# Performance work log

Measured on AMD Instinct MI355X. Metric: run time of the kernel, lower is better.

Reference implementation:

```python
import jax, jax.numpy as jnp
import numpy as np

GRID_SIZE, SPLINE_ORDER = 5, 3
NUM_BASES = GRID_SIZE + SPLINE_ORDER  # 8
GRID = jnp.asarray(np.arange(-SPLINE_ORDER, GRID_SIZE + SPLINE_ORDER + 1, dtype=np.float32) * (2.0 / GRID_SIZE) - 1.0)  # (12,)


def _b_splines(x):
    # x: (M, F) -> (M, F, NUM_BASES), Cox-de Boor recursion on shared uniform grid
    g = GRID
    xe = x[..., None]
    b = ((xe >= g[:-1]) & (xe < g[1:])).astype(x.dtype)
    for k in range(1, SPLINE_ORDER + 1):
        b = ((xe - g[:-(k + 1)]) / (g[k:-1] - g[:-(k + 1)]) * b[..., :-1]
             + (g[k + 1:] - xe) / (g[k + 1:] - g[1:-k]) * b[..., 1:])
    return b


def _kan_linear(x, base_w, spline_w):
    # x: (M, Fin); base_w: (Fout, Fin); spline_w: (Fout, Fin, NUM_BASES)
    base = jax.nn.silu(x) @ base_w.T
    spl = _b_splines(x).reshape(x.shape[0], -1) @ spline_w.reshape(spline_w.shape[0], -1).T
    return base + spl


def _ln(x, g, b, eps=1e-5):
    mu = jnp.mean(x, -1, keepdims=True)
    var = jnp.var(x, -1, keepdims=True)
    return (x - mu) * jax.lax.rsqrt(var + eps) * g + b


def _dwconv(img, w, b):
    C = img.shape[1]
    out = jax.lax.conv_general_dilated(img, w, (1, 1), 'SAME',
        dimension_numbers=('NCHW', 'OIHW', 'NCHW'), feature_group_count=C)
    return out + b[None, :, None, None]


def _dw_bn_relu(x, H, W, w, b, gamma, beta, eps=1e-5):
    # BN in eval mode with running_mean=0, running_var=1
    B, N, C = x.shape
    img = x.transpose(0, 2, 1).reshape(B, C, H, W)
    out = _dwconv(img, w, b)
    out = out * (gamma * (1.0 / np.sqrt(1.0 + eps)))[None, :, None, None] + beta[None, :, None, None]
    out = jax.nn.relu(out)
    return out.reshape(B, C, H * W).transpose(0, 2, 1)


def _cross_selective_scan(img, x_proj_w, dt_w, dt_b, A_logs, Ds, g, b):
    # img: (B, Di, H, W). 4-direction diagonal/antidiagonal selective scan (VMamba-style).
    B, Di, H, W = img.shape
    L = H * W
    K = x_proj_w.shape[0]
    R = dt_w.shape[2]
    Nst = A_logs.shape[1]
    i = jnp.arange(H)[:, None]
    j = jnp.arange(W)[None, :]
    diag = (i + j) % W
    adiag = (j - i) % W
    diag_inv = (jnp.arange(W)[None, :] - i) % W
    adiag_inv = (jnp.arange(W)[None, :] + i) % W

    def gather(x, idx):
        gth = jnp.take_along_axis(x, idx[None, None], axis=3)  # (B,Di,H,W)
        return gth.transpose(0, 1, 3, 2).reshape(B, Di, L)

    def scatter(flat, idx_inv):
        v = flat.reshape(B, Di, W, H).transpose(0, 1, 3, 2)
        return jnp.take_along_axis(v, idx_inv[None, None], axis=3)

    gd, gad = gather(img, diag), gather(img, adiag)
    xs = jnp.stack([gd, gad, jnp.flip(gd, -1), jnp.flip(gad, -1)], axis=1)  # (B,K,Di,L)
    x_dbl = jnp.einsum('bkdl,kcd->bkcl', xs, x_proj_w)
    dts, Bs, Cs = jnp.split(x_dbl, [R, R + Nst], axis=2)  # (B,K,R,L),(B,K,N,L),(B,K,N,L)
    dts = jnp.einsum('bkrl,kdr->bkdl', dts, dt_w)
    delta = jax.nn.softplus(dts + dt_b[None, :, :, None])  # (B,K,Di,L)
    A = -jnp.exp(A_logs).reshape(K, Di, Nst)

    def step(hst, inp):
        u_t, d_t, B_t, C_t = inp  # (B,K,Di),(B,K,Di),(B,K,N),(B,K,N)
        dA = jnp.exp(d_t[..., None] * A)
        hst = dA * hst + (d_t * u_t)[..., None] * B_t[:, :, None, :]
        return hst, jnp.einsum('bkdn,bkn->bkd', hst, C_t)

    h0 = jnp.zeros((B, K, Di, Nst), img.dtype)
    _, ys = jax.lax.scan(step, h0,
        (xs.transpose(3, 0, 1, 2), delta.transpose(3, 0, 1, 2),
         Bs.transpose(3, 0, 1, 2), Cs.transpose(3, 0, 1, 2)))  # ys: (L,B,K,Di)
    ys = ys.transpose(1, 2, 3, 0) + Ds.reshape(K, Di)[None, :, :, None] * xs  # (B,K,Di,L)
    yd = ys[:, 0] + jnp.flip(ys[:, 2], -1)
    ya = ys[:, 1] + jnp.flip(ys[:, 3], -1)
    y = scatter(yd, diag_inv) + scatter(ya, adiag_inv)  # (B,Di,H,W)
    y = y.reshape(B, Di, L).transpose(0, 2, 1)
    return _ln(y, g, b)  # (B,L,Di)


def setup_inputs():
    key = jax.random.key(0)
    ks = iter(jax.random.split(key, 48))
    B, H, W, C = 4, 64, 64, 96
    Di, K, Nst = 2 * C, 4, 16
    R = int(np.ceil(C / 16))
    L = H * W

    def rn(shape, s=0.05):
        return jax.random.normal(next(ks), shape, jnp.float32) * s

    return dict(
        x=jax.random.normal(next(ks), (B, L, C), jnp.float32),
        H=H, W=W,
        norm1_g=jnp.ones((C,), jnp.float32), norm1_b=jnp.zeros((C,), jnp.float32),
        in_proj_w=rn((2 * Di, C)),
        conv_w=rn((Di, 1, 3, 3), 0.2), conv_b=jnp.zeros((Di,), jnp.float32),
        x_proj_w=rn((K, R + 2 * Nst, Di)),
        dt_w=rn((K, Di, R), 0.1), dt_b=rn((K, Di), 0.1),
        A_logs=jax.random.uniform(next(ks), (K * Di, Nst), jnp.float32),
        Ds=jnp.ones((K * Di,), jnp.float32),
        out_norm_g=jnp.ones((Di,), jnp.float32), out_norm_b=jnp.zeros((Di,), jnp.float32),
        out_proj_w=rn((C, Di)),
        norm2_g=jnp.ones((C,), jnp.float32), norm2_b=jnp.zeros((C,), jnp.float32),
        fc1_base_w=rn((C, C)), fc1_spline_w=rn((C, C, NUM_BASES), 0.02),
        fc2_base_w=rn((C, C)), fc2_spline_w=rn((C, C, NUM_BASES), 0.02),
        fc3_base_w=rn((C, C)), fc3_spline_w=rn((C, C, NUM_BASES), 0.02),
        dw1_w=rn((C, 1, 3, 3), 0.2), dw1_b=jnp.zeros((C,), jnp.float32),
        dw1_g=jnp.ones((C,), jnp.float32), dw1_beta=jnp.zeros((C,), jnp.float32),
        dw2_w=rn((C, 1, 3, 3), 0.2), dw2_b=jnp.zeros((C,), jnp.float32),
        dw2_g=jnp.ones((C,), jnp.float32), dw2_beta=jnp.zeros((C,), jnp.float32),
        dw3_w=rn((C, 1, 3, 3), 0.2), dw3_b=jnp.zeros((C,), jnp.float32),
        dw3_g=jnp.ones((C,), jnp.float32), dw3_beta=jnp.zeros((C,), jnp.float32),
    )


def reference(x, H, W, norm1_g, norm1_b, in_proj_w, conv_w, conv_b, x_proj_w,
              dt_w, dt_b, A_logs, Ds, out_norm_g, out_norm_b, out_proj_w,
              norm2_g, norm2_b, fc1_base_w, fc1_spline_w, fc2_base_w, fc2_spline_w,
              fc3_base_w, fc3_spline_w, dw1_w, dw1_b, dw1_g, dw1_beta,
              dw2_w, dw2_b, dw2_g, dw2_beta, dw3_w, dw3_b, dw3_g, dw3_beta):
    B, L, C = x.shape
    # --- SS2D branch ---
    h = _ln(x, norm1_g, norm1_b)
    xz = h @ in_proj_w.T  # (B,L,2*Di)
    Di = xz.shape[-1] // 2
    xin, z = xz[..., :Di], xz[..., Di:]
    img = xin.transpose(0, 2, 1).reshape(B, Di, H, W)
    img = jax.nn.silu(_dwconv(img, conv_w, conv_b))
    y = _cross_selective_scan(img, x_proj_w, dt_w, dt_b, A_logs, Ds, out_norm_g, out_norm_b)
    y = y * jax.nn.silu(z)
    x = x + y @ out_proj_w.T
    # --- KAN branch ---
    h = _ln(x, norm2_g, norm2_b)
    M = B * L
    t = _kan_linear(h.reshape(M, C), fc1_base_w, fc1_spline_w).reshape(B, L, -1)
    t = _dw_bn_relu(t, H, W, dw1_w, dw1_b, dw1_g, dw1_beta)
    t = _kan_linear(t.reshape(M, -1), fc2_base_w, fc2_spline_w).reshape(B, L, -1)
    t = _dw_bn_relu(t, H, W, dw2_w, dw2_b, dw2_g, dw2_beta)
    t = _kan_linear(t.reshape(M, -1), fc3_base_w, fc3_spline_w).reshape(B, L, -1)
    t = _dw_bn_relu(t, H, W, dw3_w, dw3_b, dw3_g, dw3_beta)
    return x + t
```

## Files before the change

kernel.cpp:

```cpp
#include <hip/hip_runtime.h>
#include <math.h>

constexpr int B_  = 4;
constexpr int H_  = 64;
constexpr int W_  = 64;
constexpr int C_  = 96;
constexpr int L_  = H_ * W_;
constexpr int DI  = 192;
constexpr int K_  = 4;
constexpr int NST = 16;
constexpr int R_  = 6;
constexpr int M_  = B_ * L_;

constexpr int NCH = 128;
constexpr int CL  = 32;
constexpr int DG  = 12;
constexpr int HS  = 8;

constexpr int KANK = 864;
constexpr int KLAY = 96 * KANK;

typedef __attribute__((ext_vector_type(8))) short short8;
typedef __attribute__((ext_vector_type(4))) float floatx4;
typedef __attribute__((ext_vector_type(4))) unsigned short ushort4v;

__device__ __forceinline__ float wave_sum64(float v) {
#pragma unroll
  for (int off = 1; off < 64; off <<= 1) v += __shfl_xor(v, off, 64);
  return v;
}

__device__ __forceinline__ float exp2_hw(float x) {
  return __builtin_amdgcn_exp2f(x);
}

__device__ __forceinline__ int pos_kl(int k, int l) {
  int ll = (k >= 2) ? (L_ - 1 - l) : l;
  int i = ll & 63;
  int j = ll >> 6;
  int col = ((k & 1) == 0) ? ((i + j) & 63) : ((j - i) & 63);
  return (i << 6) + col;
}

__device__ __forceinline__ int pos_pair(int pr, int ll) {
  int i = ll & 63, j = ll >> 6;
  int col = (pr == 0) ? ((i + j) & 63) : ((j - i) & 63);
  return (i << 6) + col;
}

__device__ __forceinline__ float silu_f(float x) {
  return x / (1.f + __expf(-x));
}

__device__ __forceinline__ float softplus_fast(float s) {
  return fmaxf(s, 0.f) + __logf(1.f + __expf(-fabsf(s)));
}

__device__ __forceinline__ unsigned short f2bf(float f) {
  unsigned u = __float_as_uint(f);
  unsigned r = (u + 0x7FFFu + ((u >> 16) & 1u)) >> 16;
  return (unsigned short)r;
}

__device__ __forceinline__ float bf2f(unsigned short h) {
  return __uint_as_float(((unsigned)h) << 16);
}

__device__ __forceinline__ void spline8(float x, float* bb ) {
#pragma unroll
  for (int i2 = 0; i2 < 11; i2++) {
    float g0 = 0.4f * i2 - 2.2f;
    float g1 = 0.4f * i2 - 1.8f;
    bb[i2] = (x >= g0 && x < g1) ? 1.f : 0.f;
  }
#pragma unroll
  for (int k2 = 1; k2 <= 3; k2++) {
    float invd = 1.f / (0.4f * k2);
#pragma unroll
    for (int i2 = 0; i2 + k2 < 11; i2++) {
      float gi   = 0.4f * i2 - 2.2f;
      float gik1 = 0.4f * (i2 + k2 + 1) - 2.2f;
      bb[i2] = (x - gi) * invd * bb[i2] + (gik1 - x) * invd * bb[i2 + 1];
    }
  }
}

__global__ __launch_bounds__(256) void ln96_kernel(const float* __restrict__ in,
    const float* __restrict__ g, const float* __restrict__ b,
    float* __restrict__ out) {
  int wave = blockIdx.x * 4 + (threadIdx.x >> 6);
  int lane = threadIdx.x & 63;
  const float* rp = in + (size_t)wave * C_;
  float v0 = rp[lane];
  float v1 = (lane < C_ - 64) ? rp[lane + 64] : 0.f;
  float s  = wave_sum64(v0 + v1);
  float s2 = wave_sum64(v0 * v0 + v1 * v1);
  float mean = s * (1.f / C_);
  float var  = s2 * (1.f / C_) - mean * mean;
  float inv  = rsqrtf(var + 1e-5f);
  float* op = out + (size_t)wave * C_;
  op[lane] = (v0 - mean) * inv * g[lane] + b[lane];
  if (lane < C_ - 64) op[lane + 64] = (v1 - mean) * inv * g[lane + 64] + b[lane + 64];
}

__global__ __launch_bounds__(256) void prep_inproj_kernel(const float* __restrict__ w,
    unsigned short* __restrict__ wio) {
  int idx = blockIdx.x * 256 + threadIdx.x;
  if (idx >= 384 * 96) return;
  float v = w[idx];
  unsigned short hh = f2bf(v);
  wio[idx] = hh;
  wio[36864 + idx] = f2bf(v - bf2f(hh));
}

__global__ __launch_bounds__(256) void prep_a2_kernel(const float* __restrict__ A_logs,
    float* __restrict__ a2g) {
  int idx = blockIdx.x * 256 + threadIdx.x;
  if (idx < K_ * DI * NST) a2g[idx] = -__expf(A_logs[idx]) * 1.44269504f;
}

__global__ __launch_bounds__(256) void gemm_in_mfma_kernel(const float* __restrict__ h,
    const unsigned short* __restrict__ wio, float* __restrict__ xin,
    float* __restrict__ z) {
  __shared__ __align__(16) unsigned short Wh[96][104];
  __shared__ __align__(16) unsigned short Wl[96][104];
  int row0 = (blockIdx.x >> 1) * 64;
  int nc0  = (blockIdx.x & 1) * 2;
  int tid = threadIdx.x;
  int wv = tid >> 6, lane = tid & 63, mrow = lane & 15, quad = lane >> 4;

  short8 ah[3], al[3];
  const float* hr = h + (size_t)(row0 + wv * 16 + mrow) * C_;
#pragma unroll
  for (int ks = 0; ks < 3; ks++) {
    float4 va = *(const float4*)&hr[ks * 32 + quad * 8];
    float4 vb = *(const float4*)&hr[ks * 32 + quad * 8 + 4];
    float f[8] = {va.x, va.y, va.z, va.w, vb.x, vb.y, vb.z, vb.w};
    short8 hh, ll;
#pragma unroll
    for (int q = 0; q < 8; q++) {
      unsigned short hv = f2bf(f[q]);
      hh[q] = (short)hv;
      ll[q] = (short)f2bf(f[q] - bf2f(hv));
    }
    ah[ks] = hh; al[ks] = ll;
  }
  for (int nci = 0; nci < 2; nci++) {
    int nc = nc0 + nci;
    if (nci) __syncthreads();
    for (int t = tid; t < 96 * 12; t += 256) {
      int j = t / 12, u = t % 12;
      *(short8*)&Wh[j][u * 8] = *(const short8*)&wio[(size_t)(nc * 96 + j) * 96 + u * 8];
      *(short8*)&Wl[j][u * 8] = *(const short8*)&wio[(size_t)(384 + nc * 96 + j) * 96 + u * 8];
    }
    __syncthreads();
    floatx4 acc[6];
#pragma unroll
    for (int q = 0; q < 6; q++) acc[q] = (floatx4)(0.f);
#pragma unroll
    for (int ks = 0; ks < 3; ks++) {
#pragma unroll
      for (int nt = 0; nt < 6; nt++) {
        short8 bh = *(const short8*)&Wh[nt * 16 + mrow][ks * 32 + quad * 8];
        short8 bl = *(const short8*)&Wl[nt * 16 + mrow][ks * 32 + quad * 8];
        acc[nt] = __builtin_amdgcn_mfma_f32_16x16x32_bf16(ah[ks], bh, acc[nt], 0, 0, 0);
        acc[nt] = __builtin_amdgcn_mfma_f32_16x16x32_bf16(al[ks], bh, acc[nt], 0, 0, 0);
        acc[nt] = __builtin_amdgcn_mfma_f32_16x16x32_bf16(ah[ks], bl, acc[nt], 0, 0, 0);
      }
    }
#pragma unroll
    for (int nt = 0; nt < 6; nt++) {
      int j = nc * 96 + nt * 16 + mrow;
#pragma unroll
      for (int rg = 0; rg < 4; rg++) {
        int row = row0 + wv * 16 + quad * 4 + rg;
        float v = acc[nt][rg];
        if (j < DI) xin[(size_t)row * DI + j] = v;
        else        z[(size_t)row * DI + (j - DI)] = v;
      }
    }
  }
}

__global__ __launch_bounds__(192) void conv_silu_kernel(const float* __restrict__ xin,
    const float* __restrict__ cw, const float* __restrict__ cb, float* __restrict__ imgT) {
  int p = blockIdx.x;
  int b = p >> 12;
  int ij = p & 4095;
  int i = ij >> 6, j = ij & 63;
  int c = threadIdx.x;
  float acc = cb[c];
#pragma unroll
  for (int di = -1; di <= 1; di++) {
    int ii = i + di;
    if (ii < 0 || ii >= H_) continue;
#pragma unroll
    for (int dj = -1; dj <= 1; dj++) {
      int jj = j + dj;
      if (jj < 0 || jj >= W_) continue;
      acc += xin[((size_t)b * L_ + ii * W_ + jj) * DI + c] * cw[c * 9 + (di + 1) * 3 + (dj + 1)];
    }
  }
  imgT[(size_t)p * DI + c] = silu_f(acc);
}

__global__ __launch_bounds__(256) void xdbl_mfma_kernel(const float* __restrict__ imgT,
    const float* __restrict__ xpw, float* __restrict__ dts_g,
    float* __restrict__ BsT, float* __restrict__ CsT) {
  __shared__ __align__(16) unsigned short Ah[64][104];
  __shared__ __align__(16) unsigned short Al[64][104];
  __shared__ __align__(16) unsigned short Wh[48][104];
  __shared__ __align__(16) unsigned short Wl[48][104];
  __shared__ int pos_s[64];

  int blk = blockIdx.x;
  int lt = blk & 63;
  int bk = blk >> 6;
  int k = bk % K_, b = bk / K_;
  int l0 = lt * 64;
  int tid = threadIdx.x;
  int wid = tid >> 6;
  int lane = tid & 63;
  int mrow = lane & 15, quad = lane >> 4;

  if (tid < 64) pos_s[tid] = pos_kl(k, l0 + tid);
  __syncthreads();

  floatx4 acc[3];
#pragma unroll
  for (int q = 0; q < 3; q++) acc[q] = (floatx4)(0.f);

  const float* img_b = imgT + (size_t)b * L_ * DI;

  for (int kc = 0; kc < 2; kc++) {
    if (kc) __syncthreads();
    for (int t = tid; t < 64 * 24; t += 256) {
      int li = t / 24, c4 = (t % 24) * 4;
      const float4 v = *(const float4*)&img_b[(size_t)pos_s[li] * DI + kc * 96 + c4];
      ushort4v h4, l4;
      float fv[4] = {v.x, v.y, v.z, v.w};
#pragma unroll
      for (int q = 0; q < 4; q++) {
        unsigned short hh = f2bf(fv[q]);
        h4[q] = hh;
        l4[q] = f2bf(fv[q] - bf2f(hh));
      }
      *(ushort4v*)&Ah[li][c4] = h4;
      *(ushort4v*)&Al[li][c4] = l4;
    }
    for (int t = tid; t < 48 * 24; t += 256) {
      int j = t / 24, c4 = (t % 24) * 4;
      ushort4v h4 = (ushort4v)0, l4 = (ushort4v)0;
      if (j < 38) {
        int c = (j < 32) ? (j + 6) : (j - 32);
        const float4 v = *(const float4*)&xpw[((size_t)(k * 38 + c)) * DI + kc * 96 + c4];
        float fv[4] = {v.x, v.y, v.z, v.w};
#pragma unroll
        for (int q = 0; q < 4; q++) {
          unsigned short hh = f2bf(fv[q]);
          h4[q] = hh;
          l4[q] = f2bf(fv[q] - bf2f(hh));
        }
      }
      *(ushort4v*)&Wh[j][c4] = h4;
      *(ushort4v*)&Wl[j][c4] = l4;
    }
    __syncthreads();
#pragma unroll
    for (int ks = 0; ks < 3; ks++) {
      short8 ah = *(const short8*)&Ah[wid * 16 + mrow][ks * 32 + quad * 8];
      short8 al = *(const short8*)&Al[wid * 16 + mrow][ks * 32 + quad * 8];
#pragma unroll
      for (int nt = 0; nt < 3; nt++) {
        short8 bh = *(const short8*)&Wh[nt * 16 + mrow][ks * 32 + quad * 8];
        short8 bl = *(const short8*)&Wl[nt * 16 + mrow][ks * 32 + quad * 8];
        acc[nt] = __builtin_amdgcn_mfma_f32_16x16x32_bf16(ah, bh, acc[nt], 0, 0, 0);
        acc[nt] = __builtin_amdgcn_mfma_f32_16x16x32_bf16(al, bh, acc[nt], 0, 0, 0);
        acc[nt] = __builtin_amdgcn_mfma_f32_16x16x32_bf16(ah, bl, acc[nt], 0, 0, 0);
      }
    }
  }
  size_t bkL = (size_t)(b * K_ + k) * L_ + l0;
#pragma unroll
  for (int rg = 0; rg < 4; rg++) {
    int grow = wid * 16 + quad * 4 + rg;
    size_t base = (bkL + grow) * NST;
    BsT[base + mrow] = acc[0][rg];
    CsT[base + mrow] = acc[1][rg];
    if (mrow < R_) dts_g[(bkL + grow) * 8 + mrow] = acc[2][rg];
  }
}

__global__ __launch_bounds__(192) void scan1_kernel(const float* __restrict__ imgT,
    const float* __restrict__ dts_g, const float* __restrict__ BsT,
    const float* __restrict__ a2g, const float* __restrict__ dtw,
    const float* __restrict__ dtb, float* __restrict__ hend,
    float* __restrict__ aprod) {
  __shared__ float bs_s[CL][NST];
  __shared__ float dt_s[CL][8];
  int blk = blockIdx.x;
  int c = blk % NCH;
  int tmp = blk / NCH;
  int k = tmp % K_, b = tmp / K_;
  int l0 = c * CL;
  int d = threadIdx.x;
  const float* img_b = imgT + (size_t)b * L_ * DI;
  {
    const float* Bs_bk = BsT + ((size_t)(b * K_ + k) * L_ + l0) * NST;
    for (int t = d; t < CL * NST; t += 192) bs_s[t >> 4][t & 15] = Bs_bk[t];
    const float* Dt = dts_g + ((size_t)(b * K_ + k) * L_ + l0) * 8;
    for (int t = d; t < CL * 8; t += 192) dt_s[t >> 3][t & 7] = Dt[t];
  }
  float A2[NST];
  {
    const floatx4* ap = (const floatx4*)(a2g + (size_t)(k * DI + d) * NST);
#pragma unroll
    for (int i = 0; i < 4; i++) {
      floatx4 v = ap[i];
      A2[4 * i] = v[0]; A2[4 * i + 1] = v[1]; A2[4 * i + 2] = v[2]; A2[4 * i + 3] = v[3];
    }
  }
  float w6[6], bias;
  {
    const float* wp = dtw + ((size_t)k * DI + d) * R_;
#pragma unroll
    for (int r = 0; r < 6; r++) w6[r] = wp[r];
    bias = dtb[k * DI + d];
  }
  float u[CL];
#pragma unroll
  for (int q = 0; q < CL; q++)
    u[q] = img_b[(size_t)pos_kl(k, l0 + q) * DI + d];
  __syncthreads();
  float dc[CL];
  float sum_dlt = 0.f;
#pragma unroll
  for (int q = 0; q < CL; q++) {
    const floatx4* dp = (const floatx4*)&dt_s[q][0];
    floatx4 d0 = dp[0], d1 = dp[1];
    float s = bias + w6[0] * d0[0] + w6[1] * d0[1] + w6[2] * d0[2]
                   + w6[3] * d0[3] + w6[4] * d1[0] + w6[5] * d1[1];
    dc[q] = softplus_fast(s);
    sum_dlt += dc[q];
  }
  float h[NST];
#pragma unroll
  for (int n = 0; n < NST; n++) h[n] = 0.f;
#pragma unroll
  for (int q = 0; q < CL; q++) {
    float du = dc[q] * u[q];
    floatx4 bsv[4];
    const floatx4* bp = (const floatx4*)&bs_s[q][0];
#pragma unroll
    for (int i = 0; i < 4; i++) bsv[i] = bp[i];
#pragma unroll
    for (int n = 0; n < NST; n++) {
      float dA = exp2_hw(dc[q] * A2[n]);
      h[n] = dA * h[n] + du * bsv[n >> 2][n & 3];
    }
  }
  size_t base = ((size_t)(b * K_ + k) * NCH + c) * (DI * NST) + d;
#pragma unroll
  for (int n = 0; n < NST; n++) {
    hend[base + (size_t)n * DI]  = h[n];
    aprod[base + (size_t)n * DI] = exp2_hw(A2[n] * sum_dlt);
  }
}

__global__ __launch_bounds__(256) void scan_carry_kernel(float* __restrict__ hend,
    const float* __restrict__ aprod) {
  constexpr int PF = 8;
  int blk = blockIdx.x;
  int part = blk % DG;
  int bk = blk / DG;
  const size_t DNS = (size_t)DI * NST;
  size_t base = (size_t)bk * NCH * DNS + (size_t)part * 256 + threadIdx.x;
  float hb[PF], ab[PF];
#pragma unroll
  for (int q = 0; q < PF; q++) {
    hb[q] = hend[base + (size_t)q * DNS];
    ab[q] = aprod[base + (size_t)q * DNS];
  }
  float carry = 0.f;
  for (int c0 = 0; c0 < NCH; c0 += PF) {
    float hn[PF], an[PF];
    if (c0 + PF < NCH) {
#pragma unroll
      for (int q = 0; q < PF; q++) {
        hn[q] = hend[base + (size_t)(c0 + PF + q) * DNS];
        an[q] = aprod[base + (size_t)(c0 + PF + q) * DNS];
      }
    } else {
#pragma unroll
      for (int q = 0; q < PF; q++) { hn[q] = 0.f; an[q] = 0.f; }
    }
#pragma unroll
    for (int q = 0; q < PF; q++) {
      hend[base + (size_t)(c0 + q) * DNS] = carry;
      carry = ab[q] * carry + hb[q];
    }
#pragma unroll
    for (int q = 0; q < PF; q++) { hb[q] = hn[q]; ab[q] = an[q]; }
  }
}

__global__ __launch_bounds__(192) void scan2_quad_kernel(const float* __restrict__ imgT,
    const float* __restrict__ dts_g, const float* __restrict__ BsT,
    const float* __restrict__ CsT, const float* __restrict__ a2g,
    const float* __restrict__ dtw, const float* __restrict__ dtb,
    const float* __restrict__ Ds, const float* __restrict__ carry_in,
    float* __restrict__ y0g, float* __restrict__ y1g,
    float* __restrict__ y2g, float* __restrict__ y3g) {
  __shared__ float bsf[CL][HS], csf[CL][HS], bsr[CL][HS], csr[CL][HS];
  __shared__ float dtf[CL][8], dtr[CL][8];
  int blk = blockIdx.x;
  int c    = blk % NCH;
  int rest = blk / NCH;
  int pr = rest & 1;
  int hf = (rest >> 1) & 1;
  int b  = rest >> 2;
  int kf = pr, kr = pr + 2;
  int n0 = hf * HS;
  int p0 = c * CL;
  int d = threadIdx.x;
  const float* img_b = imgT + (size_t)b * L_ * DI;
  {
    const float* Bf = BsT + ((size_t)(b * K_ + kf) * L_ + p0) * NST;
    const float* Cf = CsT + ((size_t)(b * K_ + kf) * L_ + p0) * NST;
    for (int t = d; t < CL * HS; t += 192) {
      int q = t >> 3, n = t & 7;
      bsf[q][n] = Bf[q * NST + n0 + n];
      csf[q][n] = Cf[q * NST + n0 + n];
    }
    const float* Br = BsT + (size_t)(b * K_ + kr) * L_ * NST;
    const float* Cr = CsT + (size_t)(b * K_ + kr) * L_ * NST;
    for (int t = d; t < CL * HS; t += 192) {
      int q = t >> 3, n = t & 7;
      size_t sr = (size_t)(L_ - 1 - p0 - q) * NST + n0 + n;
      bsr[q][n] = Br[sr];
      csr[q][n] = Cr[sr];
    }
    const float* Df = dts_g + ((size_t)(b * K_ + kf) * L_ + p0) * 8;
    for (int t = d; t < CL * 8; t += 192) dtf[t >> 3][t & 7] = Df[t];
    const float* Dr = dts_g + (size_t)(b * K_ + kr) * L_ * 8;
    for (int t = d; t < CL * 8; t += 192) {
      int q = t >> 3, r = t & 7;
      dtr[q][r] = Dr[(size_t)(L_ - 1 - p0 - q) * 8 + r];
    }
  }
  float u[CL], y[CL];
#pragma unroll
  for (int q = 0; q < CL; q++)
    u[q] = img_b[(size_t)pos_pair(pr, p0 + q) * DI + d];
  float dsum = 0.f;
  if (pr == 0 && hf == 0)
    dsum = Ds[d] + Ds[DI + d] + Ds[2 * DI + d] + Ds[3 * DI + d];
#pragma unroll
  for (int q = 0; q < CL; q++) y[q] = dsum * u[q];
  __syncthreads();
  float A2[HS], h[HS], w6[6], bias, dc[CL];
  {
    const float* ap = a2g + (size_t)(kf * DI + d) * NST + n0;
#pragma unroll
    for (int n = 0; n < HS; n++) A2[n] = ap[n];
    size_t cb = ((size_t)(b * K_ + kf) * NCH + c) * (DI * NST) + (size_t)n0 * DI + d;
#pragma unroll
    for (int n = 0; n < HS; n++) h[n] = carry_in[cb + (size_t)n * DI];
    const float* wp = dtw + ((size_t)kf * DI + d) * R_;
#pragma unroll
    for (int r = 0; r < 6; r++) w6[r] = wp[r];
    bias = dtb[kf * DI + d];
  }
#pragma unroll
  for (int q = 0; q < CL; q++) {
    const floatx4* dp = (const floatx4*)&dtf[q][0];
    floatx4 d0 = dp[0], d1 = dp[1];
    float s = bias + w6[0] * d0[0] + w6[1] * d0[1] + w6[2] * d0[2]
                   + w6[3] * d0[3] + w6[4] * d1[0] + w6[5] * d1[1];
    dc[q] = softplus_fast(s);
  }
#pragma unroll
  for (int q = 0; q < CL; q++) {
    float du = dc[q] * u[q];
    float yq = y[q];
#pragma unroll
    for (int n = 0; n < HS; n++) {
      float dA = exp2_hw(dc[q] * A2[n]);
      h[n] = dA * h[n] + du * bsf[q][n];
      yq += h[n] * csf[q][n];
    }
    y[q] = yq;
  }
  {
    const float* ap = a2g + (size_t)(kr * DI + d) * NST + n0;
#pragma unroll
    for (int n = 0; n < HS; n++) A2[n] = ap[n];
    size_t cb = ((size_t)(b * K_ + kr) * NCH + (NCH - 1 - c)) * (DI * NST)
                + (size_t)n0 * DI + d;
#pragma unroll
    for (int n = 0; n < HS; n++) h[n] = carry_in[cb + (size_t)n * DI];
    const float* wp = dtw + ((size_t)kr * DI + d) * R_;
#pragma unroll
    for (int r = 0; r < 6; r++) w6[r] = wp[r];
    bias = dtb[kr * DI + d];
  }
#pragma unroll
  for (int q = 0; q < CL; q++) {
    const floatx4* dp = (const floatx4*)&dtr[q][0];
    floatx4 d0 = dp[0], d1 = dp[1];
    float s = bias + w6[0] * d0[0] + w6[1] * d0[1] + w6[2] * d0[2]
                   + w6[3] * d0[3] + w6[4] * d1[0] + w6[5] * d1[1];
    dc[q] = softplus_fast(s);
  }
#pragma unroll
  for (int qq = 0; qq < CL; qq++) {
    int q = CL - 1 - qq;
    float du = dc[q] * u[q];
    float yq = y[q];
#pragma unroll
    for (int n = 0; n < HS; n++) {
      float dA = exp2_hw(dc[q] * A2[n]);
      h[n] = dA * h[n] + du * bsr[q][n];
      yq += h[n] * csr[q][n];
    }
    y[q] = yq;
  }
  float* yout = (hf == 0) ? ((pr == 0) ? y0g : y1g) : ((pr == 0) ? y2g : y3g);
#pragma unroll
  for (int q = 0; q < CL; q++)
    yout[((size_t)b * L_ + pos_pair(pr, p0 + q)) * DI + d] = y[q];
}

__global__ __launch_bounds__(256) void ln_mulz_kernel(const float* __restrict__ y0g,
    const float* __restrict__ y1g, const float* __restrict__ y2g,
    const float* __restrict__ y3g, const float* __restrict__ g,
    const float* __restrict__ bb, float* __restrict__ z) {
  int wave = blockIdx.x * 4 + (threadIdx.x >> 6);
  int lane = threadIdx.x & 63;
  size_t base = (size_t)wave * DI;
  float v[3];
#pragma unroll
  for (int q = 0; q < 3; q++) {
    size_t idx = base + lane + 64 * q;
    v[q] = y0g[idx] + y1g[idx] + y2g[idx] + y3g[idx];
  }
  float s  = wave_sum64(v[0] + v[1] + v[2]);
  float s2 = wave_sum64(v[0] * v[0] + v[1] * v[1] + v[2] * v[2]);
  float mean = s * (1.f / DI);
  float var  = s2 * (1.f / DI) - mean * mean;
  float inv  = rsqrtf(var + 1e-5f);
  float* zp = z + base;
#pragma unroll
  for (int q = 0; q < 3; q++) {
    int c = lane + 64 * q;
    float zv = zp[c];
    zp[c] = ((v[q] - mean) * inv * g[c] + bb[c]) * silu_f(zv);
  }
}

__global__ __launch_bounds__(128) void outproj_kernel(const float* __restrict__ yz,
    const float* __restrict__ opw, const float* __restrict__ x, float* __restrict__ x_res) {
  __shared__ float ys[8][DI];
  int row0 = blockIdx.x * 8;
  for (int t = threadIdx.x; t < 8 * DI; t += 128)
    ys[t / DI][t % DI] = yz[(size_t)(row0 + t / DI) * DI + (t % DI)];
  __syncthreads();
  int j = threadIdx.x;
  if (j < C_) {
    float acc[8];
#pragma unroll
    for (int r = 0; r < 8; r++) acc[r] = 0.f;
    const float* wr = opw + (size_t)j * DI;
    for (int d = 0; d < DI; d++) {
      float wv = wr[d];
#pragma unroll
      for (int r = 0; r < 8; r++) acc[r] += wv * ys[r][d];
    }
#pragma unroll
    for (int r = 0; r < 8; r++) {
      size_t row = row0 + r;
      x_res[row * C_ + j] = x[row * C_ + j] + acc[r];
    }
  }
}

__global__ __launch_bounds__(256) void prepw_kernel(const float* __restrict__ bw1,
    const float* __restrict__ sw1, const float* __restrict__ bw2,
    const float* __restrict__ sw2, const float* __restrict__ bw3,
    const float* __restrict__ sw3, unsigned short* __restrict__ wcat) {
  int idx = blockIdx.x * 256 + threadIdx.x;
  if (idx >= 3 * KLAY) return;
  int layer = idx / KLAY, rem = idx % KLAY;
  int j = rem / KANK, k = rem % KANK;
  const float* bw = (layer == 0) ? bw1 : (layer == 1) ? bw2 : bw3;
  const float* sw = (layer == 0) ? sw1 : (layer == 1) ? sw2 : sw3;
  float v = (k < C_) ? bw[j * C_ + k] : sw[j * 768 + (k - C_)];
  wcat[idx] = f2bf(v);
}

__global__ __launch_bounds__(256) void kan_mfma_kernel(const float* __restrict__ in,
    const unsigned short* __restrict__ wl, float* __restrict__ out) {
  __shared__ __align__(16) float x_s[32][100];
  __shared__ __align__(16) unsigned short A_s[32][104];
  __shared__ __align__(16) unsigned short W_s[96][104];
  int row0 = blockIdx.x * 32;
  int tid = threadIdx.x;
  for (int t = tid; t < 32 * 24; t += 256) {
    int r = t / 24, c4 = (t % 24) * 4;
    *(float4*)&x_s[r][c4] = *(const float4*)&in[(size_t)(row0 + r) * C_ + c4];
  }
  floatx4 acc[3];
#pragma unroll
  for (int q = 0; q < 3; q++) acc[q] = (floatx4)(0.f);
  int wv = tid >> 6;
  int rh = wv >> 1, ch = wv & 1;
  int lane = tid & 63;
  int mrow = lane & 15, quad = lane >> 4;
  __syncthreads();
  for (int ci = 0; ci < 9; ci++) {
    if (ci) __syncthreads();
    for (int t = tid; t < 96 * 12; t += 256) {
      int j = t / 12, u = t % 12;
      *(short8*)&W_s[j][u * 8] =
          *(const short8*)&wl[(size_t)j * KANK + ci * 96 + u * 8];
    }
    if (ci == 0) {
      for (int t = tid; t < 32 * 48; t += 256) {
        int r = t / 48, k2 = (t % 48) * 2;
        unsigned v = (unsigned)f2bf(silu_f(x_s[r][k2])) |
                     ((unsigned)f2bf(silu_f(x_s[r][k2 + 1])) << 16);
        *(unsigned*)&A_s[r][k2] = v;
      }
    } else {
      int c0 = (ci - 1) * 12;
      for (int t = tid; t < 32 * 12; t += 256) {
        int r = t & 31, cl = t >> 5;
        float x = x_s[r][c0 + cl];
        float bb[11];
        spline8(x, bb);
        short8 av;
#pragma unroll
        for (int q = 0; q < 8; q++) av[q] = (short)f2bf(bb[q]);
        *(short8*)&A_s[r][cl * 8] = av;
      }
    }
    __syncthreads();
#pragma unroll
    for (int ks = 0; ks < 3; ks++) {
      short8 a = *(const short8*)&A_s[rh * 16 + mrow][ks * 32 + quad * 8];
#pragma unroll
      for (int ct = 0; ct < 3; ct++) {
        short8 b = *(const short8*)&W_s[ch * 48 + ct * 16 + mrow][ks * 32 + quad * 8];
        acc[ct] = __builtin_amdgcn_mfma_f32_16x16x32_bf16(a, b, acc[ct], 0, 0, 0);
      }
    }
  }
#pragma unroll
  for (int ct = 0; ct < 3; ct++)
#pragma unroll
    for (int rg = 0; rg < 4; rg++) {
      int row = row0 + rh * 16 + quad * 4 + rg;
      out[(size_t)row * C_ + ch * 48 + ct * 16 + mrow] = acc[ct][rg];
    }
}

__global__ __launch_bounds__(192) void dwbn_kernel(const float* __restrict__ t,
    const float* __restrict__ w, const float* __restrict__ bias,
    const float* __restrict__ gamma, const float* __restrict__ beta,
    const float* __restrict__ addres, float* __restrict__ out) {
  int tid = threadIdx.x;
  int half = (tid >= 96) ? 1 : 0;
  int c = tid - half * 96;
  int p = blockIdx.x * 2 + half;
  int b = p >> 12;
  int ij = p & 4095;
  int i = ij >> 6, j = ij & 63;
  float acc = bias[c];
#pragma unroll
  for (int di = -1; di <= 1; di++) {
    int ii = i + di;
    if (ii < 0 || ii >= H_) continue;
#pragma unroll
    for (int dj = -1; dj <= 1; dj++) {
      int jj = j + dj;
      if (jj < 0 || jj >= W_) continue;
      acc += t[((size_t)b * L_ + ii * W_ + jj) * C_ + c] * w[c * 9 + (di + 1) * 3 + (dj + 1)];
    }
  }
  float v = acc * (gamma[c] * rsqrtf(1.f + 1e-5f)) + beta[c];
  v = fmaxf(v, 0.f);
  if (addres != nullptr) v += addres[(size_t)p * C_ + c];
  out[(size_t)p * C_ + c] = v;
}

extern "C" void kernel_launch(void* const* d_in, const int* in_sizes, int n_in,
                              void* d_out, int out_size, void* d_ws, size_t ws_size,
                              hipStream_t stream) {
  const float* x         = (const float*)d_in[0];
  const float* norm1_g   = (const float*)d_in[3];
  const float* norm1_b   = (const float*)d_in[4];
  const float* in_proj_w = (const float*)d_in[5];
  const float* conv_w    = (const float*)d_in[6];
  const float* conv_b    = (const float*)d_in[7];
  const float* x_proj_w  = (const float*)d_in[8];
  const float* dt_w      = (const float*)d_in[9];
  const float* dt_b      = (const float*)d_in[10];
  const float* A_logs    = (const float*)d_in[11];
  const float* Ds        = (const float*)d_in[12];
  const float* out_ng    = (const float*)d_in[13];
  const float* out_nb    = (const float*)d_in[14];
  const float* out_proj_w= (const float*)d_in[15];
  const float* norm2_g   = (const float*)d_in[16];
  const float* norm2_b   = (const float*)d_in[17];
  const float* fc1_bw    = (const float*)d_in[18];
  const float* fc1_sw    = (const float*)d_in[19];
  const float* fc2_bw    = (const float*)d_in[20];
  const float* fc2_sw    = (const float*)d_in[21];
  const float* fc3_bw    = (const float*)d_in[22];
  const float* fc3_sw    = (const float*)d_in[23];
  const float* dw1_w     = (const float*)d_in[24];
  const float* dw1_b     = (const float*)d_in[25];
  const float* dw1_g     = (const float*)d_in[26];
  const float* dw1_be    = (const float*)d_in[27];
  const float* dw2_w     = (const float*)d_in[28];
  const float* dw2_b     = (const float*)d_in[29];
  const float* dw2_g     = (const float*)d_in[30];
  const float* dw2_be    = (const float*)d_in[31];
  const float* dw3_w     = (const float*)d_in[32];
  const float* dw3_b     = (const float*)d_in[33];
  const float* dw3_g     = (const float*)d_in[34];
  const float* dw3_be    = (const float*)d_in[35];

  float* ws = (float*)d_ws;
  float* h_buf   = ws;
  float* xin_buf = h_buf + (size_t)M_ * C_;
  float* z_buf   = xin_buf + (size_t)M_ * DI;
  float* imgT    = z_buf + (size_t)M_ * DI;
  float* BsT     = imgT + (size_t)M_ * DI;
  float* CsT     = BsT + (size_t)B_ * K_ * L_ * NST;
  float* y_pre   = CsT + (size_t)B_ * K_ * L_ * NST;
  float* x_res   = y_pre + (size_t)M_ * DI;
  float* t_a     = x_res + (size_t)M_ * C_;
  float* t_b     = t_a + (size_t)M_ * C_;
  float* hend    = t_b + (size_t)M_ * C_;
  float* aprod   = hend + (size_t)B_ * K_ * NCH * DI * NST;
  float* a2_buf  = aprod + (size_t)B_ * K_ * NCH * DI * NST;
  float* dts_g   = t_a;
  unsigned short* wio  = (unsigned short*)t_b;
  float* y1_buf  = xin_buf;
  float* y2_buf  = aprod;
  float* y3_buf  = aprod + (size_t)M_ * DI;
  unsigned short* wcat = (unsigned short*)BsT;

  ln96_kernel<<<M_ / 4, 256, 0, stream>>>(x, norm1_g, norm1_b, h_buf);
  prep_inproj_kernel<<<144, 256, 0, stream>>>(in_proj_w, wio);
  prep_a2_kernel<<<48, 256, 0, stream>>>(A_logs, a2_buf);
  gemm_in_mfma_kernel<<<(M_ / 64) * 2, 256, 0, stream>>>(h_buf, wio, xin_buf, z_buf);
  conv_silu_kernel<<<M_, 192, 0, stream>>>(xin_buf, conv_w, conv_b, imgT);
  xdbl_mfma_kernel<<<B_ * K_ * (L_ / 64), 256, 0, stream>>>(imgT, x_proj_w, dts_g,
                                                            BsT, CsT);
  scan1_kernel<<<B_ * K_ * NCH, 192, 0, stream>>>(imgT, dts_g, BsT, a2_buf,
                                                  dt_w, dt_b, hend, aprod);
  scan_carry_kernel<<<B_ * K_ * DG, 256, 0, stream>>>(hend, aprod);
  scan2_quad_kernel<<<B_ * 4 * NCH, 192, 0, stream>>>(imgT, dts_g, BsT, CsT, a2_buf,
                                                      dt_w, dt_b, Ds, hend,
                                                      y_pre, y1_buf, y2_buf, y3_buf);
  prepw_kernel<<<(3 * KLAY + 255) / 256, 256, 0, stream>>>(fc1_bw, fc1_sw, fc2_bw,
                                                           fc2_sw, fc3_bw, fc3_sw, wcat);
  ln_mulz_kernel<<<M_ / 4, 256, 0, stream>>>(y_pre, y1_buf, y2_buf, y3_buf,
                                             out_ng, out_nb, z_buf);
  outproj_kernel<<<M_ / 8, 128, 0, stream>>>(z_buf, out_proj_w, x, x_res);
  ln96_kernel<<<M_ / 4, 256, 0, stream>>>(x_res, norm2_g, norm2_b, h_buf);
  kan_mfma_kernel<<<M_ / 32, 256, 0, stream>>>(h_buf, wcat, t_a);
  dwbn_kernel<<<M_ / 2, 192, 0, stream>>>(t_a, dw1_w, dw1_b, dw1_g, dw1_be, nullptr, t_b);
  kan_mfma_kernel<<<M_ / 32, 256, 0, stream>>>(t_b, wcat + KLAY, t_a);
  dwbn_kernel<<<M_ / 2, 192, 0, stream>>>(t_a, dw2_w, dw2_b, dw2_g, dw2_be, nullptr, t_b);
  kan_mfma_kernel<<<M_ / 32, 256, 0, stream>>>(t_b, wcat + 2 * KLAY, t_a);
  dwbn_kernel<<<M_ / 2, 192, 0, stream>>>(t_a, dw3_w, dw3_b, dw3_g, dw3_be, x_res, (float*)d_out);
}
```

Before: 493.2 us.

## Restructure scan2 to one block per direction with full state dimension

```diff
diff --git a/kernel.cpp b/kernel.cpp
--- a/kernel.cpp
+++ b/kernel.cpp
@@ -15,7 +15,6 @@
 constexpr int NCH = 128;
 constexpr int CL  = 32;
 constexpr int DG  = 12;
-constexpr int HS  = 8;
 
 constexpr int KANK = 864;
 constexpr int KLAY = 96 * KANK;
@@ -39,12 +38,6 @@
   int i = ll & 63;
   int j = ll >> 6;
   int col = ((k & 1) == 0) ? ((i + j) & 63) : ((j - i) & 63);
-  return (i << 6) + col;
-}
-
-__device__ __forceinline__ int pos_pair(int pr, int ll) {
-  int i = ll & 63, j = ll >> 6;
-  int col = (pr == 0) ? ((i + j) & 63) : ((j - i) & 63);
   return (i << 6) + col;
 }
 
@@ -404,131 +397,91 @@
   }
 }
 
-__global__ __launch_bounds__(192) void scan2_quad_kernel(const float* __restrict__ imgT,
+__global__ __launch_bounds__(192) void scan2_dir_kernel(const float* __restrict__ imgT,
     const float* __restrict__ dts_g, const float* __restrict__ BsT,
     const float* __restrict__ CsT, const float* __restrict__ a2g,
     const float* __restrict__ dtw, const float* __restrict__ dtb,
     const float* __restrict__ Ds, const float* __restrict__ carry_in,
     float* __restrict__ y0g, float* __restrict__ y1g,
     float* __restrict__ y2g, float* __restrict__ y3g) {
-  __shared__ float bsf[CL][HS], csf[CL][HS], bsr[CL][HS], csr[CL][HS];
-  __shared__ float dtf[CL][8], dtr[CL][8];
+  __shared__ float bs_s[CL][NST];
+  __shared__ float cs_s[CL][NST];
+  __shared__ float dt_s[CL][8];
+  __shared__ int pos_s[CL];
   int blk = blockIdx.x;
-  int c    = blk % NCH;
-  int rest = blk / NCH;
-  int pr = rest & 1;
-  int hf = (rest >> 1) & 1;
-  int b  = rest >> 2;
-  int kf = pr, kr = pr + 2;
-  int n0 = hf * HS;
-  int p0 = c * CL;
+  int c = blk % NCH;
+  int tmp = blk / NCH;
+  int k = tmp % K_, b = tmp / K_;
+  int l0 = c * CL;
   int d = threadIdx.x;
   const float* img_b = imgT + (size_t)b * L_ * DI;
   {
-    const float* Bf = BsT + ((size_t)(b * K_ + kf) * L_ + p0) * NST;
-    const float* Cf = CsT + ((size_t)(b * K_ + kf) * L_ + p0) * NST;
-    for (int t = d; t < CL * HS; t += 192) {
-      int q = t >> 3, n = t & 7;
-      bsf[q][n] = Bf[q * NST + n0 + n];
-      csf[q][n] = Cf[q * NST + n0 + n];
-    }
-    const float* Br = BsT + (size_t)(b * K_ + kr) * L_ * NST;
-    const float* Cr = CsT + (size_t)(b * K_ + kr) * L_ * NST;
-    for (int t = d; t < CL * HS; t += 192) {
-      int q = t >> 3, n = t & 7;
-      size_t sr = (size_t)(L_ - 1 - p0 - q) * NST + n0 + n;
-      bsr[q][n] = Br[sr];
-      csr[q][n] = Cr[sr];
-    }
-    const float* Df = dts_g + ((size_t)(b * K_ + kf) * L_ + p0) * 8;
-    for (int t = d; t < CL * 8; t += 192) dtf[t >> 3][t & 7] = Df[t];
-    const float* Dr = dts_g + (size_t)(b * K_ + kr) * L_ * 8;
-    for (int t = d; t < CL * 8; t += 192) {
-      int q = t >> 3, r = t & 7;
-      dtr[q][r] = Dr[(size_t)(L_ - 1 - p0 - q) * 8 + r];
-    }
-  }
-  float u[CL], y[CL];
+    const float* Bs_bk = BsT + ((size_t)(b * K_ + k) * L_ + l0) * NST;
+    const float* Cs_bk = CsT + ((size_t)(b * K_ + k) * L_ + l0) * NST;
+    for (int t = d; t < CL * NST; t += 192) {
+      bs_s[t >> 4][t & 15] = Bs_bk[t];
+      cs_s[t >> 4][t & 15] = Cs_bk[t];
+    }
+    const float* Dt = dts_g + ((size_t)(b * K_ + k) * L_ + l0) * 8;
+    for (int t = d; t < CL * 8; t += 192) dt_s[t >> 3][t & 7] = Dt[t];
+    if (d < CL) pos_s[d] = pos_kl(k, l0 + d);
+  }
+  float A2[NST];
+  {
+    const floatx4* ap = (const floatx4*)(a2g + (size_t)(k * DI + d) * NST);
+#pragma unroll
+    for (int i = 0; i < 4; i++) {
+      floatx4 v = ap[i];
+      A2[4 * i] = v[0]; A2[4 * i + 1] = v[1]; A2[4 * i + 2] = v[2]; A2[4 * i + 3] = v[3];
+    }
+  }
+  float w6[6], bias;
+  {
+    const float* wp = dtw + ((size_t)k * DI + d) * R_;
+#pragma unroll
+    for (int r = 0; r < 6; r++) w6[r] = wp[r];
+    bias = dtb[k * DI + d];
+  }
+  float h[NST];
+  {
+    size_t cb = ((size_t)(b * K_ + k) * NCH + c) * (DI * NST) + d;
+#pragma unroll
+    for (int n = 0; n < NST; n++) h[n] = carry_in[cb + (size_t)n * DI];
+  }
+  float dsk = Ds[k * DI + d];
+  __syncthreads();
+  float u[CL];
 #pragma unroll
   for (int q = 0; q < CL; q++)
-    u[q] = img_b[(size_t)pos_pair(pr, p0 + q) * DI + d];
-  float dsum = 0.f;
-  if (pr == 0 && hf == 0)
-    dsum = Ds[d] + Ds[DI + d] + Ds[2 * DI + d] + Ds[3 * DI + d];
-#pragma unroll
-  for (int q = 0; q < CL; q++) y[q] = dsum * u[q];
-  __syncthreads();
-  float A2[HS], h[HS], w6[6], bias, dc[CL];
-  {
-    const float* ap = a2g + (size_t)(kf * DI + d) * NST + n0;
-#pragma unroll
-    for (int n = 0; n < HS; n++) A2[n] = ap[n];
-    size_t cb = ((size_t)(b * K_ + kf) * NCH + c) * (DI * NST) + (size_t)n0 * DI + d;
-#pragma unroll
-    for (int n = 0; n < HS; n++) h[n] = carry_in[cb + (size_t)n * DI];
-    const float* wp = dtw + ((size_t)kf * DI + d) * R_;
-#pragma unroll
-    for (int r = 0; r < 6; r++) w6[r] = wp[r];
-    bias = dtb[kf * DI + d];
-  }
+    u[q] = img_b[(size_t)pos_s[q] * DI + d];
+  float dc[CL];
 #pragma unroll
   for (int q = 0; q < CL; q++) {
-    const floatx4* dp = (const floatx4*)&dtf[q][0];
+    const floatx4* dp = (const floatx4*)&dt_s[q][0];
     floatx4 d0 = dp[0], d1 = dp[1];
     float s = bias + w6[0] * d0[0] + w6[1] * d0[1] + w6[2] * d0[2]
                    + w6[3] * d0[3] + w6[4] * d1[0] + w6[5] * d1[1];
     dc[q] = softplus_fast(s);
   }
+  float* yout = (k == 0) ? y0g : (k == 1) ? y1g : (k == 2) ? y2g : y3g;
+  float* y_b = yout + (size_t)b * L_ * DI;
 #pragma unroll
   for (int q = 0; q < CL; q++) {
     float du = dc[q] * u[q];
-    float yq = y[q];
-#pragma unroll
-    for (int n = 0; n < HS; n++) {
+    floatx4 bsv[4], csv[4];
+    const floatx4* bp = (const floatx4*)&bs_s[q][0];
+    const floatx4* cp = (const floatx4*)&cs_s[q][0];
+#pragma unroll
+    for (int i = 0; i < 4; i++) { bsv[i] = bp[i]; csv[i] = cp[i]; }
+    float yq = dsk * u[q];
+#pragma unroll
+    for (int n = 0; n < NST; n++) {
       float dA = exp2_hw(dc[q] * A2[n]);
-      h[n] = dA * h[n] + du * bsf[q][n];
-      yq += h[n] * csf[q][n];
-    }
-    y[q] = yq;
-  }
-  {
-    const float* ap = a2g + (size_t)(kr * DI + d) * NST + n0;
-#pragma unroll
-    for (int n = 0; n < HS; n++) A2[n] = ap[n];
-    size_t cb = ((size_t)(b * K_ + kr) * NCH + (NCH - 1 - c)) * (DI * NST)
-                + (size_t)n0 * DI + d;
-#pragma unroll
-    for (int n = 0; n < HS; n++) h[n] = carry_in[cb + (size_t)n * DI];
-    const float* wp = dtw + ((size_t)kr * DI + d) * R_;
-#pragma unroll
-    for (int r = 0; r < 6; r++) w6[r] = wp[r];
-    bias = dtb[kr * DI + d];
-  }
-#pragma unroll
-  for (int q = 0; q < CL; q++) {
-    const floatx4* dp = (const floatx4*)&dtr[q][0];
-    floatx4 d0 = dp[0], d1 = dp[1];
-    float s = bias + w6[0] * d0[0] + w6[1] * d0[1] + w6[2] * d0[2]
-                   + w6[3] * d0[3] + w6[4] * d1[0] + w6[5] * d1[1];
-    dc[q] = softplus_fast(s);
-  }
-#pragma unroll
-  for (int qq = 0; qq < CL; qq++) {
-    int q = CL - 1 - qq;
-    float du = dc[q] * u[q];
-    float yq = y[q];
-#pragma unroll
-    for (int n = 0; n < HS; n++) {
-      float dA = exp2_hw(dc[q] * A2[n]);
-      h[n] = dA * h[n] + du * bsr[q][n];
-      yq += h[n] * csr[q][n];
-    }
-    y[q] = yq;
-  }
-  float* yout = (hf == 0) ? ((pr == 0) ? y0g : y1g) : ((pr == 0) ? y2g : y3g);
-#pragma unroll
-  for (int q = 0; q < CL; q++)
-    yout[((size_t)b * L_ + pos_pair(pr, p0 + q)) * DI + d] = y[q];
+      h[n] = dA * h[n] + du * bsv[n >> 2][n & 3];
+      yq += h[n] * csv[n >> 2][n & 3];
+    }
+    y_b[(size_t)pos_s[q] * DI + d] = yq;
+  }
 }
 
 __global__ __launch_bounds__(256) void ln_mulz_kernel(const float* __restrict__ y0g,
@@ -762,7 +715,7 @@
   scan1_kernel<<<B_ * K_ * NCH, 192, 0, stream>>>(imgT, dts_g, BsT, a2_buf,
                                                   dt_w, dt_b, hend, aprod);
   scan_carry_kernel<<<B_ * K_ * DG, 256, 0, stream>>>(hend, aprod);
-  scan2_quad_kernel<<<B_ * 4 * NCH, 192, 0, stream>>>(imgT, dts_g, BsT, CsT, a2_buf,
+  scan2_dir_kernel<<<B_ * K_ * NCH, 192, 0, stream>>>(imgT, dts_g, BsT, CsT, a2_buf,
                                                       dt_w, dt_b, Ds, hend,
                                                       y_pre, y1_buf, y2_buf, y3_buf);
   prepw_kernel<<<(3 * KLAY + 255) / 256, 256, 0, stream>>>(fc1_bw, fc1_sw, fc2_bw,
```

New measurement: 528.8 us. 1.07x slower.
